# Optimization experiments

Hardware: AMD Instinct MI355X
Metric: run time of the kernel (lower is better)

Reference implementation:

```python
import jax, jax.numpy as jnp
import numpy as np
from jax import lax

N_STATE = 1024
N_HEAD = 16
H_DIM = N_STATE // N_HEAD  # 64
NUM_ROT = 8
BASE = 10000.0
B, S = 4, 4096


def setup_inputs() -> dict:
    key = jax.random.key(0)
    k1, k2, k3 = jax.random.split(key, 3)
    x = jax.random.normal(k1, (B, S, N_STATE), dtype=jnp.float32)
    thetas = jax.random.normal(k2, (NUM_ROT,), dtype=jnp.float32) * 0.1
    # torch: torch.rand(num_rotations, 2) * h_dim -> floats in [0, h_dim)
    rotation_pairs = jax.random.uniform(k3, (NUM_ROT, 2), dtype=jnp.float32) * H_DIM
    theta_scale = jnp.ones((1,), dtype=jnp.float32)
    rotation_matrix = jnp.eye(H_DIM, dtype=jnp.float32)
    inv_freq = 1.0 / BASE ** (jnp.arange(0, H_DIM, 2, dtype=jnp.float32) / H_DIM)
    return {"x": x, "thetas": thetas, "rotation_pairs": rotation_pairs,
            "theta_scale": theta_scale, "rotation_matrix": rotation_matrix,
            "inv_freq": inv_freq}


def _compose_rotation(thetas, idx, theta_scale, rotation_matrix, dtype):
    """Compose all Givens rotations + final learned rotation into one [h,h] matrix.
    Matmul is associative, so R = G_0 @ G_1 @ ... @ G_{K-1} @ rotation_matrix,
    then x @ R equals the original sequential (x @ G_k) loop."""
    eye = jnp.eye(H_DIM, dtype=dtype)

    def step(R, inp):
        i, j, theta = inp
        c, s = jnp.cos(theta), jnp.sin(theta)
        # sequential .at sets replicate torch's in-place assignment order
        G = eye.at[i, i].set(c).at[i, j].set(-s).at[j, i].set(s).at[j, j].set(c)
        return R @ G, None

    R, _ = lax.scan(step, eye, (idx[:, 0], idx[:, 1], thetas * theta_scale[0]))
    return R @ rotation_matrix


def reference(x, thetas, rotation_pairs, theta_scale, rotation_matrix, inv_freq):
    b, s, n_state = x.shape
    idx = rotation_pairs.astype(jnp.int32)  # torch .long() truncation of positive floats
    R = _compose_rotation(thetas, idx, theta_scale, rotation_matrix, x.dtype)
    xh = x.reshape(b, s, N_HEAD, H_DIM) @ R  # [b,s,h,d] @ [d,d]
    # rotary sin/cos
    pos = jnp.arange(s, dtype=inv_freq.dtype)
    sinusoid = pos[:, None] * inv_freq[None, :]          # [s, d/2]
    sin = jnp.sin(sinusoid)[None, :, None, :]
    cos = jnp.cos(sinusoid)[None, :, None, :]
    x1, x2 = xh[..., ::2], xh[..., 1::2]
    out = jnp.concatenate([x1 * cos - x2 * sin, x1 * sin + x2 * cos], axis=-1)
    return out.reshape(b, s, n_state)
```

## Files before the change

### kernel.cpp

```cpp
#include <hip/hip_runtime.h>
#include <hip/hip_bf16.h>
#include <math.h>

#define N_STATE 1024
#define N_HEAD  16
#define H_DIM   64
#define NUM_ROT 8
#define SEQ     4096
#define HVPB    128

typedef __attribute__((ext_vector_type(8))) short bf16x8;
typedef __attribute__((ext_vector_type(4))) float f32x4;

__device__ __forceinline__ unsigned short f2bf(float f) {
    union { float f; unsigned u; } v; v.f = f;
    unsigned r = v.u + 0x7fffu + ((v.u >> 16) & 1u);
    return (unsigned short)(r >> 16);
}

#define RF_STRIDE 68
#define RT_STRIDE 72
#define SM_TOTAL 44160

__global__ __launch_bounds__(256)
void rope_fused_kernel(const float* __restrict__ x,
                       const float* __restrict__ thetas,
                       const float* __restrict__ pairs,
                       const float* __restrict__ theta_scale,
                       const float* __restrict__ M,
                       const float* __restrict__ inv_freq,
                       float* __restrict__ out)
{
    __shared__ __align__(16) char smem[SM_TOTAL];
    float*          Rf   = (float*)(smem);
    float*          Ms   = (float*)(smem + 17408);
    unsigned short* Rt_s = (unsigned short*)(smem + 34816);
    float*          csh  = (float*)(smem + 44032);
    int*            prs  = (int*)(smem + 44096);
    float*          snc  = (float*)(smem);
    unsigned short* xs   = (unsigned short*)(smem + 2048);

    const int t   = threadIdx.x;
    const int w   = t >> 6;
    const int l   = t & 63;
    const int r16 = l & 15;
    const int q4  = l >> 4;
    const long long hv_base = (long long)blockIdx.x * HVPB;

    {
        const float4* Mg = (const float4*)M;
        #pragma unroll
        for (int q = 0; q < 4; ++q) {
            const int c   = t + q * 256;
            const int row = c >> 4;
            const int c4  = c & 15;
            *(float4*)&Ms[row * RF_STRIDE + c4 * 4] = Mg[c];
        }
    }
    #pragma unroll
    for (int q = 0; q < 17; ++q) Rf[t + q * 256] = 0.0f;
    if (t < NUM_ROT) {
        float sv, cv;
        sincosf(thetas[t] * theta_scale[0], &sv, &cv);
        csh[2 * t] = cv; csh[2 * t + 1] = sv;
    }
    if (t < 2 * NUM_ROT) prs[t] = (int)pairs[t];
    __syncthreads();

    if (t < H_DIM) {
        float* myrow = &Rf[t * RF_STRIDE];
        myrow[t] = 1.0f;
        #pragma unroll
        for (int k = 0; k < NUM_ROT; ++k) {
            const int   i = prs[2 * k], j = prs[2 * k + 1];
            const float c = csh[2 * k], s = csh[2 * k + 1];
            const float ri = myrow[i], rj = myrow[j];
            if (i == j) {
                myrow[i] = c * ri;
            } else {
                myrow[i] =  c * ri + s * rj;
                myrow[j] = -s * ri + c * rj;
            }
        }
    }
    __syncthreads();

    {
        bf16x8 ca[2];
        #pragma unroll
        for (int kh = 0; kh < 2; ++kh) {
            const int k2b = kh * 32 + q4 * 8;
            const int f   = w * 16 + r16;
            bf16x8 a;
            #pragma unroll
            for (int e = 0; e < 8; ++e)
                a[e] = (short)f2bf(Ms[(k2b + e) * RF_STRIDE + f]);
            ca[kh] = a;
        }
        f32x4 dacc[4];
        #pragma unroll
        for (int j = 0; j < 4; ++j) {
            f32x4 z = {0.f, 0.f, 0.f, 0.f};
            #pragma unroll
            for (int kh = 0; kh < 2; ++kh) {
                const float* rp = &Rf[(j * 16 + r16) * RF_STRIDE + kh * 32 + q4 * 8];
                const float4 f0 = *(const float4*)(rp);
                const float4 f1 = *(const float4*)(rp + 4);
                bf16x8 b;
                b[0] = (short)f2bf(f0.x); b[1] = (short)f2bf(f0.y);
                b[2] = (short)f2bf(f0.z); b[3] = (short)f2bf(f0.w);
                b[4] = (short)f2bf(f1.x); b[5] = (short)f2bf(f1.y);
                b[6] = (short)f2bf(f1.z); b[7] = (short)f2bf(f1.w);
                z = __builtin_amdgcn_mfma_f32_16x16x32_bf16(ca[kh], b, z, 0, 0, 0);
            }
            dacc[j] = z;
        }
        #pragma unroll
        for (int j = 0; j < 4; ++j) {
            #pragma unroll
            for (int r = 0; r < 4; ++r) {
                const int f = w * 16 + q4 * 4 + r;
                const int p = ((f & 1) << 5) | (f >> 1);
                Rt_s[p * RT_STRIDE + j * 16 + r16] = f2bf(dacc[j][r]);
            }
        }
    }

    const int srl = t >> 5;
    const int sf  = t & 31;
    float sv_, cv_;
    {
        const int pos = (int)(((hv_base >> 4) + srl) & (SEQ - 1));
        sincosf((float)pos * inv_freq[sf], &sv_, &cv_);
    }
    __syncthreads();

    snc[srl * 64 + sf]      = sv_;
    snc[srl * 64 + 32 + sf] = cv_;

    bf16x8 afr[4][2];
    #pragma unroll
    for (int mt = 0; mt < 4; ++mt)
        #pragma unroll
        for (int kh = 0; kh < 2; ++kh)
            afr[mt][kh] = *(const bf16x8*)(
                &Rt_s[(mt * 16 + r16) * RT_STRIDE + kh * 32 + q4 * 8]);
    __syncthreads();

    unsigned short* xw = &xs[w * 16 * RT_STRIDE];

    #pragma unroll
    for (int nt = 0; nt < 2; ++nt) {
        const size_t row0 = (size_t)(hv_base + w * 32 + nt * 16);

        {
            const float4* xg = (const float4*)(x + row0 * H_DIM);
            #pragma unroll
            for (int i = 0; i < 4; ++i) {
                const int flat = i * 64 + l;
                const float4 v = xg[flat];
                const int row = flat >> 4;
                const int c4  = flat & 15;
                ushort4 b;
                b.x = f2bf(v.x); b.y = f2bf(v.y);
                b.z = f2bf(v.z); b.w = f2bf(v.w);
                *(ushort4*)(&xw[row * RT_STRIDE + c4 * 4]) = b;
            }
        }

        f32x4 acc[4];
        {
            bf16x8 b0 = *(const bf16x8*)(&xw[r16 * RT_STRIDE + 0 * 32 + q4 * 8]);
            bf16x8 b1 = *(const bf16x8*)(&xw[r16 * RT_STRIDE + 1 * 32 + q4 * 8]);
            #pragma unroll
            for (int mt = 0; mt < 4; ++mt) {
                f32x4 z = {0.0f, 0.0f, 0.0f, 0.0f};
                z = __builtin_amdgcn_mfma_f32_16x16x32_bf16(afr[mt][0], b0, z, 0, 0, 0);
                z = __builtin_amdgcn_mfma_f32_16x16x32_bf16(afr[mt][1], b1, z, 0, 0, 0);
                acc[mt] = z;
            }
        }

        const int pl = w * 2 + nt;
        float* op = out + row0 * H_DIM + (size_t)r16 * H_DIM;

        #pragma unroll
        for (int half = 0; half < 2; ++half) {
            const int p0 = half * 16 + q4 * 4;
            const float4 sn = *(const float4*)(&snc[pl * 64 + p0]);
            const float4 cs = *(const float4*)(&snc[pl * 64 + 32 + p0]);
            const f32x4 a1 = acc[half];
            const f32x4 a2 = acc[half + 2];
            float4 olo, ohi;
            olo.x = a1.x * cs.x - a2.x * sn.x;
            olo.y = a1.y * cs.y - a2.y * sn.y;
            olo.z = a1.z * cs.z - a2.z * sn.z;
            olo.w = a1.w * cs.w - a2.w * sn.w;
            ohi.x = a1.x * sn.x + a2.x * cs.x;
            ohi.y = a1.y * sn.y + a2.y * cs.y;
            ohi.z = a1.z * sn.z + a2.z * cs.z;
            ohi.w = a1.w * sn.w + a2.w * cs.w;
            *(float4*)(op + p0)      = olo;
            *(float4*)(op + 32 + p0) = ohi;
        }
    }
}

extern "C" void kernel_launch(void* const* d_in, const int* in_sizes, int n_in,
                              void* d_out, int out_size, void* d_ws, size_t ws_size,
                              hipStream_t stream)
{
    const float* x      = (const float*)d_in[0];
    const float* thetas = (const float*)d_in[1];
    const float* pairs  = (const float*)d_in[2];
    const float* tscale = (const float*)d_in[3];
    const float* M      = (const float*)d_in[4];
    const float* invf   = (const float*)d_in[5];
    float* out = (float*)d_out;

    const int n_hv   = in_sizes[0] / H_DIM;
    const int blocks = n_hv / HVPB;
    rope_fused_kernel<<<blocks, 256, 0, stream>>>(x, thetas, pairs, tscale,
                                                  M, invf, out);
}
```

Measured before the change: 32.81 us.

## Process two strided tiles per block with register prefetch of x

```diff
diff --git a/kernel.cpp b/kernel.cpp
--- a/kernel.cpp
+++ b/kernel.cpp
@@ -8,6 +8,7 @@
 #define NUM_ROT 8
 #define SEQ     4096
 #define HVPB    128
+#define TILES   2
 
 typedef __attribute__((ext_vector_type(8))) short bf16x8;
 typedef __attribute__((ext_vector_type(4))) float f32x4;
@@ -20,51 +21,48 @@
 
 #define RF_STRIDE 68
 #define RT_STRIDE 72
-#define SM_TOTAL 44160
-
-__global__ __launch_bounds__(256)
+#define SM_TOTAL 26752
+
+__global__ __launch_bounds__(256, 4)
 void rope_fused_kernel(const float* __restrict__ x,
                        const float* __restrict__ thetas,
                        const float* __restrict__ pairs,
                        const float* __restrict__ theta_scale,
                        const float* __restrict__ M,
                        const float* __restrict__ inv_freq,
-                       float* __restrict__ out)
+                       float* __restrict__ out,
+                       int nb)
 {
     __shared__ __align__(16) char smem[SM_TOTAL];
     float*          Rf   = (float*)(smem);
-    float*          Ms   = (float*)(smem + 17408);
-    unsigned short* Rt_s = (unsigned short*)(smem + 34816);
-    float*          csh  = (float*)(smem + 44032);
-    int*            prs  = (int*)(smem + 44096);
+    unsigned short* Rt_s = (unsigned short*)(smem + 17408);
+    float*          csh  = (float*)(smem + 26624);
+    int*            prs  = (int*)(smem + 26688);
     float*          snc  = (float*)(smem);
-    unsigned short* xs   = (unsigned short*)(smem + 2048);
+    unsigned short* xs   = (unsigned short*)(smem + 4096);
 
     const int t   = threadIdx.x;
     const int w   = t >> 6;
     const int l   = t & 63;
     const int r16 = l & 15;
     const int q4  = l >> 4;
-    const long long hv_base = (long long)blockIdx.x * HVPB;
-
-    {
-        const float4* Mg = (const float4*)M;
-        #pragma unroll
-        for (int q = 0; q < 4; ++q) {
-            const int c   = t + q * 256;
-            const int row = c >> 4;
-            const int c4  = c & 15;
-            *(float4*)&Ms[row * RF_STRIDE + c4 * 4] = Mg[c];
-        }
-    }
-    #pragma unroll
-    for (int q = 0; q < 17; ++q) Rf[t + q * 256] = 0.0f;
+    const int bid = blockIdx.x;
+
+    float am[2][8];
+    #pragma unroll
+    for (int kh = 0; kh < 2; ++kh)
+        #pragma unroll
+        for (int e = 0; e < 8; ++e)
+            am[kh][e] = M[(kh * 32 + q4 * 8 + e) * H_DIM + w * 16 + r16];
+
     if (t < NUM_ROT) {
         float sv, cv;
         sincosf(thetas[t] * theta_scale[0], &sv, &cv);
         csh[2 * t] = cv; csh[2 * t + 1] = sv;
     }
     if (t < 2 * NUM_ROT) prs[t] = (int)pairs[t];
+    #pragma unroll
+    for (int q = 0; q < 17; ++q) Rf[t + q * 256] = 0.0f;
     __syncthreads();
 
     if (t < H_DIM) {
@@ -89,12 +87,9 @@
         bf16x8 ca[2];
         #pragma unroll
         for (int kh = 0; kh < 2; ++kh) {
-            const int k2b = kh * 32 + q4 * 8;
-            const int f   = w * 16 + r16;
             bf16x8 a;
             #pragma unroll
-            for (int e = 0; e < 8; ++e)
-                a[e] = (short)f2bf(Ms[(k2b + e) * RF_STRIDE + f]);
+            for (int e = 0; e < 8; ++e) a[e] = (short)f2bf(am[kh][e]);
             ca[kh] = a;
         }
         f32x4 dacc[4];
@@ -128,16 +123,22 @@
 
     const int srl = t >> 5;
     const int sf  = t & 31;
-    float sv_, cv_;
+    float svv[TILES], cvv[TILES];
     {
-        const int pos = (int)(((hv_base >> 4) + srl) & (SEQ - 1));
-        sincosf((float)pos * inv_freq[sf], &sv_, &cv_);
-    }
-    __syncthreads();
-
-    snc[srl * 64 + sf]      = sv_;
-    snc[srl * 64 + 32 + sf] = cv_;
-
+        const float fr = inv_freq[sf];
+        #pragma unroll
+        for (int tt = 0; tt < TILES; ++tt) {
+            const int pos = ((bid + tt * nb) * 8 + srl) & (SEQ - 1);
+            sincosf((float)pos * fr, &svv[tt], &cvv[tt]);
+        }
+    }
+    __syncthreads();
+
+    #pragma unroll
+    for (int tt = 0; tt < TILES; ++tt) {
+        snc[tt * 512 + srl * 64 + sf]      = svv[tt];
+        snc[tt * 512 + srl * 64 + 32 + sf] = cvv[tt];
+    }
     bf16x8 afr[4][2];
     #pragma unroll
     for (int mt = 0; mt < 4; ++mt)
@@ -149,29 +150,41 @@
 
     unsigned short* xw = &xs[w * 16 * RT_STRIDE];
 
-    #pragma unroll
-    for (int nt = 0; nt < 2; ++nt) {
-        const size_t row0 = (size_t)(hv_base + w * 32 + nt * 16);
-
-        {
-            const float4* xg = (const float4*)(x + row0 * H_DIM);
-            #pragma unroll
-            for (int i = 0; i < 4; ++i) {
-                const int flat = i * 64 + l;
-                const float4 v = xg[flat];
-                const int row = flat >> 4;
-                const int c4  = flat & 15;
-                ushort4 b;
-                b.x = f2bf(v.x); b.y = f2bf(v.y);
-                b.z = f2bf(v.z); b.w = f2bf(v.w);
-                *(ushort4*)(&xw[row * RT_STRIDE + c4 * 4]) = b;
-            }
+    float4 cur[4], nxt[4];
+    {
+        const size_t row0 = (size_t)bid * HVPB + w * 32;
+        const float4* xg = (const float4*)(x + row0 * H_DIM);
+        #pragma unroll
+        for (int i = 0; i < 4; ++i) cur[i] = xg[i * 64 + l];
+    }
+
+    #pragma unroll
+    for (int c = 0; c < 2 * TILES; ++c) {
+        const int tt = c >> 1, nt = c & 1;
+        const size_t row0 = (size_t)(bid + tt * nb) * HVPB + w * 32 + nt * 16;
+
+        if (c + 1 < 2 * TILES) {
+            const int tt2 = (c + 1) >> 1, nt2 = (c + 1) & 1;
+            const size_t r2 = (size_t)(bid + tt2 * nb) * HVPB + w * 32 + nt2 * 16;
+            const float4* xg = (const float4*)(x + r2 * H_DIM);
+            #pragma unroll
+            for (int i = 0; i < 4; ++i) nxt[i] = xg[i * 64 + l];
+        }
+
+        #pragma unroll
+        for (int i = 0; i < 4; ++i) {
+            const int flat = i * 64 + l;
+            const int row = flat >> 4, c4 = flat & 15;
+            ushort4 b;
+            b.x = f2bf(cur[i].x); b.y = f2bf(cur[i].y);
+            b.z = f2bf(cur[i].z); b.w = f2bf(cur[i].w);
+            *(ushort4*)(&xw[row * RT_STRIDE + c4 * 4]) = b;
         }
 
         f32x4 acc[4];
         {
-            bf16x8 b0 = *(const bf16x8*)(&xw[r16 * RT_STRIDE + 0 * 32 + q4 * 8]);
-            bf16x8 b1 = *(const bf16x8*)(&xw[r16 * RT_STRIDE + 1 * 32 + q4 * 8]);
+            bf16x8 b0 = *(const bf16x8*)(&xw[r16 * RT_STRIDE + q4 * 8]);
+            bf16x8 b1 = *(const bf16x8*)(&xw[r16 * RT_STRIDE + 32 + q4 * 8]);
             #pragma unroll
             for (int mt = 0; mt < 4; ++mt) {
                 f32x4 z = {0.0f, 0.0f, 0.0f, 0.0f};
@@ -181,14 +194,13 @@
             }
         }
 
-        const int pl = w * 2 + nt;
+        const int pl = tt * 512 + (w * 2 + nt) * 64;
         float* op = out + row0 * H_DIM + (size_t)r16 * H_DIM;
-
         #pragma unroll
         for (int half = 0; half < 2; ++half) {
             const int p0 = half * 16 + q4 * 4;
-            const float4 sn = *(const float4*)(&snc[pl * 64 + p0]);
-            const float4 cs = *(const float4*)(&snc[pl * 64 + 32 + p0]);
+            const float4 sn = *(const float4*)(&snc[pl + p0]);
+            const float4 cs = *(const float4*)(&snc[pl + 32 + p0]);
             const f32x4 a1 = acc[half];
             const f32x4 a2 = acc[half + 2];
             float4 olo, ohi;
@@ -203,6 +215,11 @@
             *(float4*)(op + p0)      = olo;
             *(float4*)(op + 32 + p0) = ohi;
         }
+
+        if (c + 1 < 2 * TILES) {
+            #pragma unroll
+            for (int i = 0; i < 4; ++i) cur[i] = nxt[i];
+        }
     }
 }
 
@@ -219,7 +236,7 @@
     float* out = (float*)d_out;
 
     const int n_hv   = in_sizes[0] / H_DIM;
-    const int blocks = n_hv / HVPB;
+    const int blocks = n_hv / (HVPB * TILES);
     rope_fused_kernel<<<blocks, 256, 0, stream>>>(x, thetas, pairs, tscale,
-                                                  M, invf, out);
+                                                  M, invf, out, blocks);
 }
```

Result: faster. 28.42 us (-13.4%).
